# Optimization experiments

Measured on AMD Instinct MI355X. Metric: run time of the kernel, lower is better.

Reference implementation:

```python
import jax, jax.numpy as jnp
import numpy as np

B, N, E = 2, 20000, 200000
IN_F, OUT_F, HEADS = 256, 32, 4
NEG_SLOPE = 0.2


def setup_inputs() -> dict:
    key = jax.random.key(0)
    k1, k2, k3, k4 = jax.random.split(key, 4)
    x = jax.random.normal(k1, (B, N, IN_F), dtype=jnp.float32)
    edge_indices = jax.random.randint(k2, (2, E), 0, N, dtype=jnp.int64)
    # xavier-uniform-like scales
    W = jax.random.normal(k3, (OUT_F * HEADS, IN_F), dtype=jnp.float32) * np.float32(1.0 / np.sqrt(IN_F))
    a = jax.random.normal(k4, (2 * OUT_F, 1), dtype=jnp.float32) * np.float32(0.1)
    return {"x": x, "edge_indices": edge_indices, "W": W, "a": a}


def reference(x, edge_indices, W, a):
    Bq, Nq, _ = x.shape
    Hh, Ff = HEADS, OUT_F
    # h: [B, N, H, F]
    h = (x @ W.T).reshape(Bq, Nq, Hh, Ff)
    src, dst = edge_indices[0], edge_indices[1]
    Eq = src.shape[0]
    h_src = h[:, src]  # [B, E, H, F]
    h_dst = h[:, dst]  # [B, E, H, F]
    # scores = leaky_relu(concat(h_src, h_dst) @ a)  without materializing concat
    a_src, a_dst = a[:Ff, 0], a[Ff:, 0]
    scores = (jnp.einsum('behf,f->beh', h_src, a_src)
              + jnp.einsum('behf,f->beh', h_dst, a_dst))
    scores = jnp.where(scores > 0, scores, NEG_SLOPE * scores)  # LeakyReLU(0.2)
    # Original applies softmax over dim=0 (the BATCH dim) per edge
    sm = jax.nn.softmax(scores, axis=0)  # [B, E, H]
    # Original loop overwrites attention_weights[:, src] per edge, so only the
    # LAST edge with a given src survives.
    edge_ids = jnp.arange(Eq, dtype=jnp.int32)
    last_edge = jax.ops.segment_max(edge_ids, src, num_segments=Nq)
    has_edge = jax.ops.segment_sum(jnp.ones((Eq,), jnp.int32), src, num_segments=Nq) > 0
    last_edge = jnp.clip(last_edge, 0, Eq - 1)
    aw = jnp.where(has_edge[None, :, None], sm[:, last_edge], 0.0)  # [B, N, H]
    # aggregated[:, s] = aw[:, s] * sum_{edges i: src[i]==s} h_dst[:, i]
    seg = jax.ops.segment_sum(jnp.transpose(h_dst, (1, 0, 2, 3)), src, num_segments=Nq)  # [N,B,H,F]
    seg = jnp.transpose(seg, (1, 0, 2, 3))  # [B, N, H, F]
    aggregated = aw[..., None] * seg
    # mean over heads; dropout is identity in eval mode
    return aggregated.mean(axis=2)  # [B, N, F]
```

## Files before the change

### kernel.cpp

```cpp
#include <hip/hip_runtime.h>
#include <hip/hip_bf16.h>

#define BB 2
#define NN 20000
#define EE 200000
#define INF 256
#define OUTF 32
#define NH 4
#define HF 128
#define NEG_SLOPE 0.2f
#define GEMM_BLOCKS 625
#define EDGE_BLOCKS 782
#define CAP 48
#define OVF_CAP 8192

using bf16 = __hip_bfloat16;
typedef __attribute__((ext_vector_type(8))) short bf16x8;
typedef __attribute__((ext_vector_type(4))) float f32x4;

__device__ __forceinline__ float bf2f(unsigned short s){ return __uint_as_float((unsigned)s << 16); }
__device__ __forceinline__ ushort f2bf_bits(float f){
    __hip_bfloat16 b = __float2bfloat16(f);
    return *(ushort*)&b;
}

__device__ __forceinline__ int get_src(const int* ei, int e, int f64){
    return f64 ? ei[2 * e] : ei[e];
}
__device__ __forceinline__ int get_dst(const int* ei, int e, int f64){
    return f64 ? ei[2 * EE + 2 * e] : ei[EE + e];
}

__global__ void k_init(const ushort* __restrict__ xr, const int* __restrict__ er,
                       const void* __restrict__ Wv,
                       int* __restrict__ flags, ushort* __restrict__ wbf,
                       int* __restrict__ cnt, int* __restrict__ last_e,
                       int* __restrict__ ovf_cnt){
    int i = blockIdx.x * blockDim.x + threadIdx.x;
    if (i < NN){ cnt[i] = 0; last_e[i] = -1; }
    if (i == 0) *ovf_cnt = 0;
    if (blockIdx.x < 16){
        __shared__ int cnt_big, cnt_nz;
        if (threadIdx.x == 0){ cnt_big = 0; cnt_nz = 0; }
        __syncthreads();
        int big = 0;
        for (int k = threadIdx.x; k < 8192; k += blockDim.x){
            unsigned e = ((unsigned)xr[2 * k] >> 7) & 0xff;
            if (e >= 0xC0) big++;
        }
        int nz = 0;
        for (int k = threadIdx.x; k < 4096; k += blockDim.x){
            if (er[2 * k + 1] != 0) nz++;
        }
        atomicAdd(&cnt_big, big);
        atomicAdd(&cnt_nz, nz);
        __syncthreads();
        if (blockIdx.x == 0 && threadIdx.x == 0){
            flags[0] = (cnt_big >= 16) ? 1 : 0;
            flags[1] = (cnt_nz == 0) ? 1 : 0;
        }
        const bool f32w = (cnt_big >= 16);
        int fr = blockIdx.x * 256 + threadIdx.x;
        {
            int lane = fr & 63;
            int t    = (fr >> 6) & 3;
            int kc   = (fr >> 8) & 7;
            int ch   = fr >> 11;
            int col  = ch * 64 + t * 16 + (lane & 15);
            int kb   = kc * 32 + (lane >> 4) * 8;
            bf16x8 v;
            if (f32w){
                const float* wg = (const float*)Wv + (size_t)col * INF + kb;
                #pragma unroll
                for (int j = 0; j < 8; ++j) v[j] = (short)f2bf_bits(wg[j]);
            } else {
                const ushort* wg = (const ushort*)Wv + (size_t)col * INF + kb;
                #pragma unroll
                for (int j = 0; j < 8; ++j) v[j] = (short)wg[j];
            }
            *(bf16x8*)(wbf + (size_t)fr * 8) = v;
        }
    }
}

__global__ __launch_bounds__(256, 2)
void k_gemm(const void* __restrict__ xv_, const ushort* __restrict__ wbf,
            const void* __restrict__ av, const int* __restrict__ ei,
            const int* __restrict__ flags, ushort* __restrict__ h,
            float* __restrict__ alpha_s, float* __restrict__ alpha_d,
            int* __restrict__ last_e, int* __restrict__ cnt,
            unsigned* __restrict__ slots, int* __restrict__ ovf_cnt,
            int* __restrict__ ovf_list){
    if (blockIdx.x < EDGE_BLOCKS){
        int f64 = flags[1];
        int e = blockIdx.x * 256 + threadIdx.x;
        if (e < EE){
            int s = get_src(ei, e, f64);
            int idx = atomicAdd(&cnt[s], 1);
            if (idx < CAP) slots[(size_t)s * CAP + idx] = (unsigned)e;
            else {
                atomicMax(&last_e[s], e);
                int o = atomicAdd(ovf_cnt, 1);
                if (o < OVF_CAP) ovf_list[o] = e;
            }
        }
        return;
    }

    const int bid  = blockIdx.x - EDGE_BLOCKS;
    const int tid  = threadIdx.x;
    const int lane = tid & 63;
    const int w    = tid >> 6;
    const int l15  = lane & 15;
    const int q    = lane >> 4;
    const bool f32 = flags[0] != 0;

    const int row0 = bid * 64 + w * 16;

    f32x4 acc[2][4];
    #pragma unroll
    for (int c = 0; c < 2; ++c)
        #pragma unroll
        for (int t = 0; t < 4; ++t) acc[c][t] = (f32x4){0.f, 0.f, 0.f, 0.f};

    if (f32){
        const float* xp = (const float*)xv_ + (size_t)(row0 + l15) * INF + q * 8;
        float4 c0 = ((const float4*)xp)[0];
        float4 c1 = ((const float4*)xp)[1];
        #pragma unroll
        for (int kc = 0; kc < 8; ++kc){
            float4 n0, n1;
            if (kc < 7){
                const float4* p = (const float4*)(xp + (kc + 1) * 32);
                n0 = p[0];
                n1 = p[1];
            }
            bf16x8 afrag;
            afrag[0] = (short)f2bf_bits(c0.x); afrag[1] = (short)f2bf_bits(c0.y);
            afrag[2] = (short)f2bf_bits(c0.z); afrag[3] = (short)f2bf_bits(c0.w);
            afrag[4] = (short)f2bf_bits(c1.x); afrag[5] = (short)f2bf_bits(c1.y);
            afrag[6] = (short)f2bf_bits(c1.z); afrag[7] = (short)f2bf_bits(c1.w);
            #pragma unroll
            for (int c = 0; c < 2; ++c){
                const ushort* wb = wbf + (size_t)c * 16384;
                #pragma unroll
                for (int t = 0; t < 4; ++t){
                    bf16x8 bfrag = *(const bf16x8*)(wb + (((size_t)kc * 4 + t) * 64 + lane) * 8);
                    acc[c][t] = __builtin_amdgcn_mfma_f32_16x16x32_bf16(afrag, bfrag, acc[c][t], 0, 0, 0);
                }
            }
            if (kc < 7){ c0 = n0; c1 = n1; }
        }
    } else {
        const ushort* xp = (const ushort*)xv_ + (size_t)(row0 + l15) * INF + q * 8;
        bf16x8 af = *(const bf16x8*)xp;
        #pragma unroll
        for (int kc = 0; kc < 8; ++kc){
            bf16x8 nf;
            if (kc < 7) nf = *(const bf16x8*)(xp + (kc + 1) * 32);
            #pragma unroll
            for (int c = 0; c < 2; ++c){
                const ushort* wb = wbf + (size_t)c * 16384;
                #pragma unroll
                for (int t = 0; t < 4; ++t){
                    bf16x8 bfrag = *(const bf16x8*)(wb + (((size_t)kc * 4 + t) * 64 + lane) * 8);
                    acc[c][t] = __builtin_amdgcn_mfma_f32_16x16x32_bf16(af, bfrag, acc[c][t], 0, 0, 0);
                }
            }
            if (kc < 7) af = nf;
        }
    }

    #pragma unroll
    for (int r = 0; r < 4; ++r){
        int row = row0 + q * 4 + r;
        #pragma unroll
        for (int t = 0; t < 2; ++t){
            unsigned v0 = (unsigned)f2bf_bits(acc[0][t][r])
                        | ((unsigned)f2bf_bits(acc[0][t + 2][r]) << 16);
            unsigned v1 = (unsigned)f2bf_bits(acc[1][t][r])
                        | ((unsigned)f2bf_bits(acc[1][t + 2][r]) << 16);
            int f = t * 16 + l15;
            uint2 vv; vv.x = v0; vv.y = v1;
            *(uint2*)(h + (size_t)row * HF + f * 4) = vv;
        }
    }

    float as_lo, as_hi, ad_lo, ad_hi;
    if (f32){
        const float* af = (const float*)av;
        as_lo = af[l15];        as_hi = af[16 + l15];
        ad_lo = af[OUTF + l15]; ad_hi = af[OUTF + 16 + l15];
    } else {
        const ushort* ab = (const ushort*)av;
        as_lo = bf2f(ab[l15]);        as_hi = bf2f(ab[16 + l15]);
        ad_lo = bf2f(ab[OUTF + l15]); ad_hi = bf2f(ab[OUTF + 16 + l15]);
    }
    #pragma unroll
    for (int r = 0; r < 4; ++r){
        int row = row0 + q * 4 + r;
        #pragma unroll
        for (int c = 0; c < 2; ++c){
            #pragma unroll
            for (int hp = 0; hp < 2; ++hp){
                int t0 = hp * 2, t1 = hp * 2 + 1;
                float ps = acc[c][t0][r] * as_lo + acc[c][t1][r] * as_hi;
                float pd = acc[c][t0][r] * ad_lo + acc[c][t1][r] * ad_hi;
                ps += __shfl_down(ps, 8, 16); pd += __shfl_down(pd, 8, 16);
                ps += __shfl_down(ps, 4, 16); pd += __shfl_down(pd, 4, 16);
                ps += __shfl_down(ps, 2, 16); pd += __shfl_down(pd, 2, 16);
                ps += __shfl_down(ps, 1, 16); pd += __shfl_down(pd, 1, 16);
                if (l15 == 0){
                    size_t o = (size_t)row * NH + c * 2 + hp;
                    alpha_s[o] = ps;
                    alpha_d[o] = pd;
                }
            }
        }
    }
}

__global__ __launch_bounds__(256)
void k_agg(const unsigned* __restrict__ slots, const int* __restrict__ cnt,
           const int* __restrict__ last_e, const int* __restrict__ ei,
           const int* __restrict__ flags,
           const float* __restrict__ alpha_s, const float* __restrict__ alpha_d,
           const ushort* __restrict__ h, float* __restrict__ aw,
           float* __restrict__ out_f){
    int lane = threadIdx.x & 63;
    int wid  = (blockIdx.x * blockDim.x + threadIdx.x) >> 6;
    int nw   = (gridDim.x * blockDim.x) >> 6;
    int b = lane >> 5;
    int f = lane & 31;
    int c  = lane & 7;
    int bb = c >> 2;
    int hh = c & 3;
    int f64 = flags[1];
    for (int n = wid; n < NN; n += nw){
        int m  = cnt[n]; if (m > CAP) m = CAP;
        int le = last_e[n];

        const unsigned* sl = slots + (size_t)n * CAP;
        const ushort* hb = h + (size_t)b * NN * HF + f * 4;
        float ax = 0.f, ay = 0.f, az = 0.f, aww = 0.f;
        int i = 0;
        for (; i + 4 <= m; i += 4){
            uint4 ee = *(const uint4*)(sl + i);
            le = max(le, (int)ee.x); le = max(le, (int)ee.y);
            le = max(le, (int)ee.z); le = max(le, (int)ee.w);
            int d0 = get_dst(ei, (int)ee.x, f64);
            int d1 = get_dst(ei, (int)ee.y, f64);
            int d2 = get_dst(ei, (int)ee.z, f64);
            int d3 = get_dst(ei, (int)ee.w, f64);
            ushort4 u0 = *(const ushort4*)(hb + (size_t)d0 * HF);
            ushort4 u1 = *(const ushort4*)(hb + (size_t)d1 * HF);
            ushort4 u2 = *(const ushort4*)(hb + (size_t)d2 * HF);
            ushort4 u3 = *(const ushort4*)(hb + (size_t)d3 * HF);
            ax += bf2f(u0.x) + bf2f(u1.x) + bf2f(u2.x) + bf2f(u3.x);
            ay += bf2f(u0.y) + bf2f(u1.y) + bf2f(u2.y) + bf2f(u3.y);
            az += bf2f(u0.z) + bf2f(u1.z) + bf2f(u2.z) + bf2f(u3.z);
            aww += bf2f(u0.w) + bf2f(u1.w) + bf2f(u2.w) + bf2f(u3.w);
        }
        for (; i < m; ++i){
            int e = (int)sl[i];
            le = max(le, e);
            int d = get_dst(ei, e, f64);
            ushort4 u = *(const ushort4*)(hb + (size_t)d * HF);
            ax += bf2f(u.x); ay += bf2f(u.y); az += bf2f(u.z); aww += bf2f(u.w);
        }

        float my_aw = 0.f;
        if (le >= 0){
            int d = get_dst(ei, le, f64);
            float ss = alpha_s[((size_t)bb * NN + n) * NH + hh]
                     + alpha_d[((size_t)bb * NN + d) * NH + hh];
            float so = alpha_s[((size_t)(1 - bb) * NN + n) * NH + hh]
                     + alpha_d[((size_t)(1 - bb) * NN + d) * NH + hh];
            ss = ss > 0.f ? ss : NEG_SLOPE * ss;
            so = so > 0.f ? so : NEG_SLOPE * so;
            float mx = fmaxf(ss, so);
            float e0 = __expf(ss - mx);
            float e1 = __expf(so - mx);
            my_aw = 0.25f * e0 / (e0 + e1);
        }
        if (lane < 8) aw[((size_t)bb * NN + n) * NH + hh] = my_aw;

        float aw0 = __shfl(my_aw, (b << 2) + 0, 8);
        float aw1 = __shfl(my_aw, (b << 2) + 1, 8);
        float aw2 = __shfl(my_aw, (b << 2) + 2, 8);
        float aw3 = __shfl(my_aw, (b << 2) + 3, 8);

        out_f[((size_t)b * NN + n) * OUTF + f] =
            aw0 * ax + aw1 * ay + aw2 * az + aw3 * aww;
    }
}

__global__ void k_fix(const int* __restrict__ ei, const int* __restrict__ flags,
                      const int* __restrict__ ovf_cnt, const int* __restrict__ ovf_list,
                      const ushort* __restrict__ h, const float* __restrict__ aw,
                      float* __restrict__ out_f){
    int lane = threadIdx.x & 63;
    int wid  = (blockIdx.x * blockDim.x + threadIdx.x) >> 6;
    int nw   = (gridDim.x * blockDim.x) >> 6;
    int b = lane >> 5;
    int f = lane & 31;
    int M = *ovf_cnt; if (M > OVF_CAP) M = OVF_CAP;
    int f64 = flags[1];
    for (int i = wid; i < M; i += nw){
        int e = ovf_list[i];
        int s = get_src(ei, e, f64);
        int d = get_dst(ei, e, f64);
        float4 awv = *(const float4*)(aw + ((size_t)b * NN + s) * NH);
        ushort4 u = *(const ushort4*)(h + ((size_t)b * NN + d) * HF + f * 4);
        float acc = awv.x * bf2f(u.x) + awv.y * bf2f(u.y)
                  + awv.z * bf2f(u.z) + awv.w * bf2f(u.w);
        atomicAdd(&out_f[((size_t)b * NN + s) * OUTF + f], acc);
    }
}

extern "C" void kernel_launch(void* const* d_in, const int* in_sizes, int n_in,
                              void* d_out, int out_size, void* d_ws, size_t ws_size,
                              hipStream_t stream){
    const void* x = d_in[0]; const void* eiv = d_in[1];
    const void* W = d_in[2]; const void* a  = d_in[3];
    for (int i = 0; i < n_in; ++i){
        if      (in_sizes[i] == BB * NN * INF) x   = d_in[i];
        else if (in_sizes[i] == 2 * EE)        eiv = d_in[i];
        else if (in_sizes[i] == HF * INF)      W   = d_in[i];
        else if (in_sizes[i] == 2 * OUTF)      a   = d_in[i];
    }
    const int* ei = (const int*)eiv;
    float* out = (float*)d_out;

    const size_t HN = (size_t)BB * NN * HF;
    char* p = (char*)d_ws;
    int*      flags    = (int*)p;                     p += 64;
    ushort*   wbf      = (ushort*)p;                  p += 32768 * 2;
    ushort*   h        = (ushort*)p;                  p += HN * 2;
    float*    alpha_s  = (float*)p;                   p += (size_t)BB * NN * NH * 4;
    float*    alpha_d  = (float*)p;                   p += (size_t)BB * NN * NH * 4;
    float*    aw       = (float*)p;                   p += (size_t)BB * NN * NH * 4;
    int*      last_e   = (int*)p;                     p += (size_t)NN * 4;
    int*      cnt      = (int*)p;                     p += (size_t)NN * 4;
    int*      ovf_cnt  = (int*)p;                     p += 64;
    int*      ovf_list = (int*)p;                     p += (size_t)OVF_CAP * 4;
    unsigned* slots    = (unsigned*)p;

    k_init <<<(NN + 255) / 256, 256, 0, stream>>>((const ushort*)x, ei, W, flags, wbf,
                                                  cnt, last_e, ovf_cnt);
    k_gemm <<<EDGE_BLOCKS + GEMM_BLOCKS, 256, 0, stream>>>(x, wbf, a, ei, flags, h,
                                                           alpha_s, alpha_d, last_e,
                                                           cnt, slots, ovf_cnt, ovf_list);
    k_agg  <<<2048, 256, 0, stream>>>(slots, cnt, last_e, ei, flags,
                                      alpha_s, alpha_d, h, aw, out);
    k_fix  <<<32, 256, 0, stream>>>(ei, flags, ovf_cnt, ovf_list, h, aw, out);
}
```

Baseline: 152.3 us.

## Fuse init, GEMM, edge bucketing and aggregation into one cooperative kernel

Replaces the four-kernel pipeline with a single cooperative persistent kernel that uses grid-wide syncs between phases: input and weight setup, then edge bucketing plus bf16 MFMA GEMM, then aggregation, then an optional overflow fix-up. Edge slots now pack (edge id + 1, dst) into 64-bit values, so the last edge per source falls out of a max over the slots instead of separate atomics. The goal is to remove kernel launch gaps and tail effects between stages. In exchange it adds grid.sync costs, runs every phase at a single occupancy-limited grid size, and each block re-runs the small format-detection scan.

```diff
diff --git a/kernel.cpp b/kernel.cpp
--- a/kernel.cpp
+++ b/kernel.cpp
@@ -1,5 +1,8 @@
 #include <hip/hip_runtime.h>
 #include <hip/hip_bf16.h>
+#include <hip/hip_cooperative_groups.h>
+
+namespace cg = cooperative_groups;
 
 #define BB 2
 #define NN 20000
@@ -17,6 +20,7 @@
 using bf16 = __hip_bfloat16;
 typedef __attribute__((ext_vector_type(8))) short bf16x8;
 typedef __attribute__((ext_vector_type(4))) float f32x4;
+typedef unsigned long long u64;
 
 __device__ __forceinline__ float bf2f(unsigned short s){ return __uint_as_float((unsigned)s << 16); }
 __device__ __forceinline__ ushort f2bf_bits(float f){
@@ -29,6 +33,285 @@
 }
 __device__ __forceinline__ int get_dst(const int* ei, int e, int f64){
     return f64 ? ei[2 * EE + 2 * e] : ei[EE + e];
+}
+
+__global__ __launch_bounds__(256, 4)
+void k_fused(const void* __restrict__ xv_, const int* __restrict__ ei,
+             const void* __restrict__ Wv, const void* __restrict__ av,
+             ushort* __restrict__ wbf, ushort* __restrict__ h,
+             float* __restrict__ alpha_s, float* __restrict__ alpha_d,
+             u64* __restrict__ last_e64, int* __restrict__ cnt,
+             u64* __restrict__ slots, int* __restrict__ ovf_cnt,
+             int* __restrict__ ovf_list, float* __restrict__ aw,
+             float* __restrict__ out_f)
+{
+    cg::grid_group grid = cg::this_grid();
+    const int tid = threadIdx.x;
+    const int nb  = gridDim.x;
+    const int gt  = blockIdx.x * 256 + tid;
+    const int nthreads = nb * 256;
+
+    __shared__ int sh_big, sh_nz;
+    if (tid == 0){ sh_big = 0; sh_nz = 0; }
+    __syncthreads();
+    {
+        const ushort* xr = (const ushort*)xv_;
+        int big = 0;
+        for (int k = tid; k < 2048; k += 256){
+            unsigned e = ((unsigned)xr[2 * k] >> 7) & 0xff;
+            if (e >= 0xC0) big++;
+        }
+        int nz = 0;
+        for (int k = tid; k < 1024; k += 256){
+            if (ei[2 * k + 1] != 0) nz++;
+        }
+        if (big) atomicAdd(&sh_big, big);
+        if (nz)  atomicAdd(&sh_nz, nz);
+    }
+    __syncthreads();
+    const bool f32 = sh_big >= 8;
+    const int  f64 = (sh_nz == 0) ? 1 : 0;
+
+    for (int i = gt; i < NN; i += nthreads){ cnt[i] = 0; last_e64[i] = 0ULL; }
+    if (gt == 0) *ovf_cnt = 0;
+
+    if (blockIdx.x < 16){
+        int fr = blockIdx.x * 256 + tid;
+        int lane = fr & 63;
+        int t    = (fr >> 6) & 3;
+        int kc   = (fr >> 8) & 7;
+        int ch   = fr >> 11;
+        int col  = ch * 64 + t * 16 + (lane & 15);
+        int kb   = kc * 32 + (lane >> 4) * 8;
+        bf16x8 v;
+        if (f32){
+            const float* wg = (const float*)Wv + (size_t)col * INF + kb;
+            #pragma unroll
+            for (int j = 0; j < 8; ++j) v[j] = (short)f2bf_bits(wg[j]);
+        } else {
+            const ushort* wg = (const ushort*)Wv + (size_t)col * INF + kb;
+            #pragma unroll
+            for (int j = 0; j < 8; ++j) v[j] = (short)wg[j];
+        }
+        *(bf16x8*)(wbf + (size_t)fr * 8) = v;
+    }
+
+    grid.sync();
+
+    for (int e = gt; e < EE; e += nthreads){
+        int s = get_src(ei, e, f64);
+        int d = get_dst(ei, e, f64);
+        u64 pk = ((u64)(unsigned)(e + 1) << 16) | (unsigned)(d & 0xFFFF);
+        int idx = atomicAdd(&cnt[s], 1);
+        if (idx < CAP) slots[(size_t)s * CAP + idx] = pk;
+        else {
+            atomicMax(&last_e64[s], pk);
+            int o = atomicAdd(ovf_cnt, 1);
+            if (o < OVF_CAP) ovf_list[o] = e;
+        }
+    }
+
+    for (int bid = blockIdx.x; bid < GEMM_BLOCKS; bid += nb){
+        const int lane = tid & 63;
+        const int w    = tid >> 6;
+        const int l15  = lane & 15;
+        const int q    = lane >> 4;
+        const int row0 = bid * 64 + w * 16;
+
+        f32x4 acc[2][4];
+        #pragma unroll
+        for (int c = 0; c < 2; ++c)
+            #pragma unroll
+            for (int t = 0; t < 4; ++t) acc[c][t] = (f32x4){0.f, 0.f, 0.f, 0.f};
+
+        if (f32){
+            const float* xp = (const float*)xv_ + (size_t)(row0 + l15) * INF + q * 8;
+            float4 c0 = ((const float4*)xp)[0];
+            float4 c1 = ((const float4*)xp)[1];
+            #pragma unroll
+            for (int kc = 0; kc < 8; ++kc){
+                float4 n0, n1;
+                if (kc < 7){
+                    const float4* p = (const float4*)(xp + (kc + 1) * 32);
+                    n0 = p[0];
+                    n1 = p[1];
+                }
+                bf16x8 afrag;
+                afrag[0] = (short)f2bf_bits(c0.x); afrag[1] = (short)f2bf_bits(c0.y);
+                afrag[2] = (short)f2bf_bits(c0.z); afrag[3] = (short)f2bf_bits(c0.w);
+                afrag[4] = (short)f2bf_bits(c1.x); afrag[5] = (short)f2bf_bits(c1.y);
+                afrag[6] = (short)f2bf_bits(c1.z); afrag[7] = (short)f2bf_bits(c1.w);
+                #pragma unroll
+                for (int c = 0; c < 2; ++c){
+                    const ushort* wb = wbf + (size_t)c * 16384;
+                    #pragma unroll
+                    for (int t = 0; t < 4; ++t){
+                        bf16x8 bfrag = *(const bf16x8*)(wb + (((size_t)kc * 4 + t) * 64 + lane) * 8);
+                        acc[c][t] = __builtin_amdgcn_mfma_f32_16x16x32_bf16(afrag, bfrag, acc[c][t], 0, 0, 0);
+                    }
+                }
+                if (kc < 7){ c0 = n0; c1 = n1; }
+            }
+        } else {
+            const ushort* xp = (const ushort*)xv_ + (size_t)(row0 + l15) * INF + q * 8;
+            bf16x8 af = *(const bf16x8*)xp;
+            #pragma unroll
+            for (int kc = 0; kc < 8; ++kc){
+                bf16x8 nf;
+                if (kc < 7) nf = *(const bf16x8*)(xp + (kc + 1) * 32);
+                #pragma unroll
+                for (int c = 0; c < 2; ++c){
+                    const ushort* wb = wbf + (size_t)c * 16384;
+                    #pragma unroll
+                    for (int t = 0; t < 4; ++t){
+                        bf16x8 bfrag = *(const bf16x8*)(wb + (((size_t)kc * 4 + t) * 64 + lane) * 8);
+                        acc[c][t] = __builtin_amdgcn_mfma_f32_16x16x32_bf16(af, bfrag, acc[c][t], 0, 0, 0);
+                    }
+                }
+                if (kc < 7) af = nf;
+            }
+        }
+
+        #pragma unroll
+        for (int r = 0; r < 4; ++r){
+            int row = row0 + q * 4 + r;
+            #pragma unroll
+            for (int t = 0; t < 2; ++t){
+                unsigned v0 = (unsigned)f2bf_bits(acc[0][t][r])
+                            | ((unsigned)f2bf_bits(acc[0][t + 2][r]) << 16);
+                unsigned v1 = (unsigned)f2bf_bits(acc[1][t][r])
+                            | ((unsigned)f2bf_bits(acc[1][t + 2][r]) << 16);
+                int f = t * 16 + l15;
+                uint2 vv; vv.x = v0; vv.y = v1;
+                *(uint2*)(h + (size_t)row * HF + f * 4) = vv;
+            }
+        }
+
+        float as_lo, as_hi, ad_lo, ad_hi;
+        if (f32){
+            const float* af = (const float*)av;
+            as_lo = af[l15];        as_hi = af[16 + l15];
+            ad_lo = af[OUTF + l15]; ad_hi = af[OUTF + 16 + l15];
+        } else {
+            const ushort* ab = (const ushort*)av;
+            as_lo = bf2f(ab[l15]);        as_hi = bf2f(ab[16 + l15]);
+            ad_lo = bf2f(ab[OUTF + l15]); ad_hi = bf2f(ab[OUTF + 16 + l15]);
+        }
+        #pragma unroll
+        for (int r = 0; r < 4; ++r){
+            int row = row0 + q * 4 + r;
+            #pragma unroll
+            for (int c = 0; c < 2; ++c){
+                #pragma unroll
+                for (int hp = 0; hp < 2; ++hp){
+                    int t0 = hp * 2, t1 = hp * 2 + 1;
+                    float ps = acc[c][t0][r] * as_lo + acc[c][t1][r] * as_hi;
+                    float pd = acc[c][t0][r] * ad_lo + acc[c][t1][r] * ad_hi;
+                    ps += __shfl_down(ps, 8, 16); pd += __shfl_down(pd, 8, 16);
+                    ps += __shfl_down(ps, 4, 16); pd += __shfl_down(pd, 4, 16);
+                    ps += __shfl_down(ps, 2, 16); pd += __shfl_down(pd, 2, 16);
+                    ps += __shfl_down(ps, 1, 16); pd += __shfl_down(pd, 1, 16);
+                    if (l15 == 0){
+                        size_t o = (size_t)row * NH + c * 2 + hp;
+                        alpha_s[o] = ps;
+                        alpha_d[o] = pd;
+                    }
+                }
+            }
+        }
+    }
+
+    grid.sync();
+
+    const int M = *ovf_cnt;
+    {
+        int lane = tid & 63;
+        int wid  = (blockIdx.x * 256 + tid) >> 6;
+        int nw   = nthreads >> 6;
+        int b = lane >> 5;
+        int f = lane & 31;
+        int c  = lane & 7;
+        int bb = c >> 2;
+        int hh = c & 3;
+        for (int n = wid; n < NN; n += nw){
+            int m = cnt[n]; if (m > CAP) m = CAP;
+            u64 le = last_e64[n];
+
+            const u64* sl = slots + (size_t)n * CAP;
+            const ushort* hb = h + (size_t)b * NN * HF + f * 4;
+            float ax = 0.f, ay = 0.f, az = 0.f, aww = 0.f;
+            int i = 0;
+            for (; i + 4 <= m; i += 4){
+                ulonglong2 p0 = *(const ulonglong2*)(sl + i);
+                ulonglong2 p1 = *(const ulonglong2*)(sl + i + 2);
+                le = p0.x > le ? p0.x : le;  le = p0.y > le ? p0.y : le;
+                le = p1.x > le ? p1.x : le;  le = p1.y > le ? p1.y : le;
+                int d0 = (int)(p0.x & 0xFFFFULL);
+                int d1 = (int)(p0.y & 0xFFFFULL);
+                int d2 = (int)(p1.x & 0xFFFFULL);
+                int d3 = (int)(p1.y & 0xFFFFULL);
+                ushort4 u0 = *(const ushort4*)(hb + (size_t)d0 * HF);
+                ushort4 u1 = *(const ushort4*)(hb + (size_t)d1 * HF);
+                ushort4 u2 = *(const ushort4*)(hb + (size_t)d2 * HF);
+                ushort4 u3 = *(const ushort4*)(hb + (size_t)d3 * HF);
+                ax += bf2f(u0.x) + bf2f(u1.x) + bf2f(u2.x) + bf2f(u3.x);
+                ay += bf2f(u0.y) + bf2f(u1.y) + bf2f(u2.y) + bf2f(u3.y);
+                az += bf2f(u0.z) + bf2f(u1.z) + bf2f(u2.z) + bf2f(u3.z);
+                aww += bf2f(u0.w) + bf2f(u1.w) + bf2f(u2.w) + bf2f(u3.w);
+            }
+            for (; i < m; ++i){
+                u64 pk = sl[i];
+                le = pk > le ? pk : le;
+                int d = (int)(pk & 0xFFFFULL);
+                ushort4 u = *(const ushort4*)(hb + (size_t)d * HF);
+                ax += bf2f(u.x); ay += bf2f(u.y); az += bf2f(u.z); aww += bf2f(u.w);
+            }
+
+            float my_aw = 0.f;
+            if (le != 0ULL){
+                int d = (int)(le & 0xFFFFULL);
+                float ss = alpha_s[((size_t)bb * NN + n) * NH + hh]
+                         + alpha_d[((size_t)bb * NN + d) * NH + hh];
+                float so = alpha_s[((size_t)(1 - bb) * NN + n) * NH + hh]
+                         + alpha_d[((size_t)(1 - bb) * NN + d) * NH + hh];
+                ss = ss > 0.f ? ss : NEG_SLOPE * ss;
+                so = so > 0.f ? so : NEG_SLOPE * so;
+                float mx = fmaxf(ss, so);
+                float e0 = __expf(ss - mx);
+                float e1 = __expf(so - mx);
+                my_aw = 0.25f * e0 / (e0 + e1);
+            }
+            if (lane < 8) aw[((size_t)bb * NN + n) * NH + hh] = my_aw;
+
+            float aw0 = __shfl(my_aw, (b << 2) + 0, 8);
+            float aw1 = __shfl(my_aw, (b << 2) + 1, 8);
+            float aw2 = __shfl(my_aw, (b << 2) + 2, 8);
+            float aw3 = __shfl(my_aw, (b << 2) + 3, 8);
+
+            out_f[((size_t)b * NN + n) * OUTF + f] =
+                aw0 * ax + aw1 * ay + aw2 * az + aw3 * aww;
+        }
+    }
+
+    if (M != 0){
+        grid.sync();
+        int Mc = M > OVF_CAP ? OVF_CAP : M;
+        int lane = tid & 63;
+        int wid  = (blockIdx.x * 256 + tid) >> 6;
+        int nw   = nthreads >> 6;
+        int b = lane >> 5;
+        int f = lane & 31;
+        for (int i = wid; i < Mc; i += nw){
+            int e = ovf_list[i];
+            int s = get_src(ei, e, f64);
+            int d = get_dst(ei, e, f64);
+            float4 awv = *(const float4*)(aw + ((size_t)b * NN + s) * NH);
+            ushort4 u = *(const ushort4*)(h + ((size_t)b * NN + d) * HF + f * 4);
+            float a2 = awv.x * bf2f(u.x) + awv.y * bf2f(u.y)
+                     + awv.z * bf2f(u.z) + awv.w * bf2f(u.w);
+            atomicAdd(&out_f[((size_t)b * NN + s) * OUTF + f], a2);
+        }
+    }
 }
 
 __global__ void k_init(const ushort* __restrict__ xr, const int* __restrict__ er,
@@ -114,7 +397,6 @@
     const int l15  = lane & 15;
     const int q    = lane >> 4;
     const bool f32 = flags[0] != 0;
-
     const int row0 = bid * 64 + w * 16;
 
     f32x4 acc[2][4];
@@ -334,24 +616,59 @@
 
     const size_t HN = (size_t)BB * NN * HF;
     char* p = (char*)d_ws;
-    int*      flags    = (int*)p;                     p += 64;
-    ushort*   wbf      = (ushort*)p;                  p += 32768 * 2;
-    ushort*   h        = (ushort*)p;                  p += HN * 2;
-    float*    alpha_s  = (float*)p;                   p += (size_t)BB * NN * NH * 4;
-    float*    alpha_d  = (float*)p;                   p += (size_t)BB * NN * NH * 4;
-    float*    aw       = (float*)p;                   p += (size_t)BB * NN * NH * 4;
-    int*      last_e   = (int*)p;                     p += (size_t)NN * 4;
-    int*      cnt      = (int*)p;                     p += (size_t)NN * 4;
-    int*      ovf_cnt  = (int*)p;                     p += 64;
-    int*      ovf_list = (int*)p;                     p += (size_t)OVF_CAP * 4;
-    unsigned* slots    = (unsigned*)p;
+    int*   flags    = (int*)p;                        p += 64;
+    ushort* wbf     = (ushort*)p;                     p += 32768 * 2;
+    ushort* h       = (ushort*)p;                     p += HN * 2;
+    float* alpha_s  = (float*)p;                      p += (size_t)BB * NN * NH * 4;
+    float* alpha_d  = (float*)p;                      p += (size_t)BB * NN * NH * 4;
+    float* aw       = (float*)p;                      p += (size_t)BB * NN * NH * 4;
+    u64*   last_e64 = (u64*)p;                        p += (size_t)NN * 8;
+    int*   cnt      = (int*)p;                        p += (size_t)NN * 4;
+    int*   ovf_cnt  = (int*)p;                        p += 64;
+    int*   ovf_list = (int*)p;                        p += (size_t)OVF_CAP * 4;
+    u64*   slots    = (u64*)p;
+
+    static int coop_state = 0;
+    static int coop_grid  = 1024;
+    if (coop_state == 0){
+        int dev = 0;
+        hipGetDevice(&dev);
+        hipDeviceProp_t prop{};
+        int occ = 0;
+        if (hipGetDeviceProperties(&prop, dev) == hipSuccess &&
+            prop.cooperativeLaunch &&
+            hipOccupancyMaxActiveBlocksPerMultiprocessor(&occ, k_fused, 256, 0) == hipSuccess &&
+            occ > 0){
+            long g = (long)occ * (long)prop.multiProcessorCount;
+            if (g > 2048) g = 2048;
+            if (g < 256)  g = 256;
+            coop_grid  = (int)g;
+            coop_state = 1;
+        } else {
+            coop_state = -1;
+        }
+    }
+
+    if (coop_state == 1){
+        void* ka[] = { (void*)&x, (void*)&ei, (void*)&W, (void*)&a,
+                       (void*)&wbf, (void*)&h, (void*)&alpha_s, (void*)&alpha_d,
+                       (void*)&last_e64, (void*)&cnt, (void*)&slots,
+                       (void*)&ovf_cnt, (void*)&ovf_list, (void*)&aw, (void*)&out };
+        hipError_t err = hipLaunchCooperativeKernel((void*)k_fused,
+                                                    dim3(coop_grid), dim3(256),
+                                                    ka, 0, stream);
+        if (err == hipSuccess) return;
+        coop_state = -1;
+    }
 
     k_init <<<(NN + 255) / 256, 256, 0, stream>>>((const ushort*)x, ei, W, flags, wbf,
-                                                  cnt, last_e, ovf_cnt);
+                                                  cnt, (int*)last_e64, ovf_cnt);
     k_gemm <<<EDGE_BLOCKS + GEMM_BLOCKS, 256, 0, stream>>>(x, wbf, a, ei, flags, h,
-                                                           alpha_s, alpha_d, last_e,
-                                                           cnt, slots, ovf_cnt, ovf_list);
-    k_agg  <<<2048, 256, 0, stream>>>(slots, cnt, last_e, ei, flags,
+                                                           alpha_s, alpha_d,
+                                                           (int*)last_e64, cnt,
+                                                           (unsigned*)slots, ovf_cnt,
+                                                           ovf_list);
+    k_agg  <<<2048, 256, 0, stream>>>((unsigned*)slots, cnt, (int*)last_e64, ei, flags,
                                       alpha_s, alpha_d, h, aw, out);
     k_fix  <<<32, 256, 0, stream>>>(ei, flags, ovf_cnt, ovf_list, h, aw, out);
 }
```

Measured after the change: 322.3 us. 2.12x slower.
